# Optimization experiments

Measured on AMD Instinct MI355X. Metric: run time of the kernel, lower is better.

Reference implementation:

```python
import jax, jax.numpy as jnp
import numpy as np

N = 2048
IMG_H = 128
IMG_W = 128
FX = 160.0
FY = 160.0
CX = IMG_W / 2.0
CY = IMG_H / 2.0
THRESH = 0.001  # matches thresh in tile_based_vol_rendering
EPS = 1e-6


def _quat_scale_to_rotmat(q, s):
    # qsvec2rotmat_batched: R(q) @ diag(s), q = (w, x, y, z)
    q = q / jnp.linalg.norm(q, axis=-1, keepdims=True)
    w, x, y, z = q[..., 0], q[..., 1], q[..., 2], q[..., 3]
    R = jnp.stack([
        jnp.stack([1 - 2 * (y * y + z * z), 2 * (x * y - w * z), 2 * (x * z + w * y)], -1),
        jnp.stack([2 * (x * y + w * z), 1 - 2 * (x * x + z * z), 2 * (y * z - w * x)], -1),
        jnp.stack([2 * (x * z - w * y), 2 * (y * z + w * x), 1 - 2 * (x * x + y * y)], -1),
    ], -2)  # [N,3,3]
    return R * s[:, None, :]  # scale columns


def _jacobian(u):
    # EWA projection Jacobian, exactly as in the torch code
    l = jnp.linalg.norm(u, axis=-1)
    x, y, z = u[..., 0], u[..., 1], u[..., 2]
    zero = jnp.zeros_like(z)
    row0 = jnp.stack([1.0 / z, zero, -x / (z * z)], -1)
    row1 = jnp.stack([zero, 1.0 / z, -y / (z * z)], -1)
    row2 = jnp.stack([x / l, y / l, z / l], -1)
    return jnp.stack([row0, row1, row2], -2)  # [N,3,3]


def _forward(mean, qvec, svec, color, alpha, c2w, H, W):
    # --- project_gaussians ---
    d = -c2w[:, 3]
    Wm = c2w[:, :3].T  # world->cam rotation
    pm = jnp.einsum('ij,bj->bi', Wm, mean + d)  # [N,3] camera-space means
    M = _quat_scale_to_rotmat(qvec, svec)
    sigma = jnp.einsum('bij,bkj->bik', M, M)  # R S S^T R^T
    J = _jacobian(pm)
    JW = jnp.einsum('bij,jk->bik', J, Wm)
    cov3 = jnp.einsum('bij,bjk,blk->bil', JW, sigma, JW)
    cov2d = cov3[:, :2, :2]  # [N,2,2]
    depth = pm[:, 2]
    mean2d = pm[:, :2] / depth[:, None]  # [N,2] camera-plane coords

    # --- global depth sort (replaces per-tile radix sort; same compositing order) ---
    order = jnp.argsort(depth)
    mean2d = jnp.take(mean2d, order, axis=0)
    cov2d = jnp.take(cov2d, order, axis=0)
    color_s = jnp.take(color, order, axis=0)
    alpha_s = jnp.take(alpha, order, axis=0)

    # --- 2x2 inverse covariance ---
    a = cov2d[:, 0, 0] + EPS
    b = cov2d[:, 0, 1]
    dd = cov2d[:, 1, 1] + EPS
    det = a * dd - b * b
    i00 = dd / det
    i01 = -b / det
    i11 = a / det

    # --- pixel centers on camera plane: topleft + pixel_size * (idx + 0.5) ---
    xs = (jnp.arange(W, dtype=mean.dtype) + 0.5) / FX - CX / FX  # [W]
    ys = (jnp.arange(H, dtype=mean.dtype) + 0.5) / FY - CY / FY  # [H]
    px = jnp.broadcast_to(xs[None, :], (H, W)).reshape(-1)  # [P]
    py = jnp.broadcast_to(ys[:, None], (H, W)).reshape(-1)  # [P]

    # --- sorted alpha compositing, dense per (pixel, gaussian) ---
    dx = px[:, None] - mean2d[None, :, 0]  # [P,N]
    dy = py[:, None] - mean2d[None, :, 1]  # [P,N]
    power = -0.5 * (i00[None, :] * dx * dx + 2.0 * i01[None, :] * dx * dy + i11[None, :] * dy * dy)
    wgt = alpha_s[None, :] * jnp.exp(power)  # [P,N]
    wgt = jnp.minimum(wgt, 0.999)
    wgt = jnp.where(wgt > THRESH, wgt, 0.0)  # CUDA kernel skip threshold
    T = jnp.cumprod(1.0 - wgt, axis=1)
    T = jnp.concatenate([jnp.ones((T.shape[0], 1), T.dtype), T[:, :-1]], axis=1)  # exclusive transmittance
    out = (wgt * T) @ color_s  # [P,3]
    return out.reshape(H, W, 3)


def setup_inputs() -> dict:
    key = jax.random.key(0)
    k1, k2, k3, k4, k5, k6 = jax.random.split(key, 6)
    z = jax.random.uniform(k1, (N,), minval=2.0, maxval=6.0)
    xy = jax.random.uniform(k2, (N, 2), minval=-0.3, maxval=0.3) * z[:, None]
    mean = jnp.concatenate([xy, z[:, None]], axis=-1).astype(jnp.float32)
    qvec = jax.random.normal(k3, (N, 4), dtype=jnp.float32)
    svec = jax.random.uniform(k4, (N, 3), minval=0.02, maxval=0.08, dtype=jnp.float32)
    color = jax.random.uniform(k5, (N, 3), dtype=jnp.float32)
    alpha = jax.random.uniform(k6, (N,), minval=0.3, maxval=0.9, dtype=jnp.float32)
    c2w = jnp.concatenate([jnp.eye(3, dtype=jnp.float32), jnp.zeros((3, 1), jnp.float32)], axis=-1)
    return {"mean": mean, "qvec": qvec, "svec": svec, "color": color,
            "alpha": alpha, "c2w": c2w, "H": IMG_H, "W": IMG_W}


def reference(mean, qvec, svec, color, alpha, c2w, H, W):
    return _forward(mean, qvec, svec, color, alpha, c2w, H, W)
```

## Files before the change

### kernel.cpp

```cpp
#include <hip/hip_runtime.h>

#define FXc 160.0f
#define FYc 160.0f
#define THRESHc 0.001f
#define EPSc 1e-6f
#define QTH 1024
#define CAP 1000

__global__ __launch_bounds__(QTH) void fused_kernel(
    const float* __restrict__ mean, const float* __restrict__ qvec,
    const float* __restrict__ svec, const float* __restrict__ color,
    const float* __restrict__ alpha, const float* __restrict__ c2w,
    const int* __restrict__ Wp, const int* __restrict__ Hp,
    float* __restrict__ out, int n) {
    __shared__ unsigned long long key[CAP];
    __shared__ int   ord[CAP];
    __shared__ float4 pp0[CAP], pp1[CAP];
    __shared__ float  ppa[CAP];
    __shared__ float4 partial[16][64];
    __shared__ int cntS;

    int tid = threadIdx.x;
    int lane = tid & 63;
    int w = tid >> 6;

    int W = *Wp, H = *Hp;
    int qpx = (W + 7) >> 3;
    int q = blockIdx.x;
    int qx = q % qpx, qy = q / qpx;
    float cxofx = (W * 0.5f) / FXc, cyofy = (H * 0.5f) / FYc;
    float wx0 = ((float)(qx*8)   + 0.5f) / FXc - cxofx;
    float wx1 = ((float)(qx*8+7) + 0.5f) / FXc - cxofx;
    float wy0 = ((float)(qy*8)   + 0.5f) / FYc - cyofy;
    float wy1 = ((float)(qy*8+7) + 0.5f) / FYc - cyofy;
    int col = qx * 8 + (lane & 7);
    int row = qy * 8 + (lane >> 3);
    float px = ((float)col + 0.5f) / FXc - cxofx;
    float py = ((float)row + 0.5f) / FYc - cyofy;

    if (tid == 0) cntS = 0;
    __syncthreads();

    float tx = c2w[3], ty = c2w[7], tz = c2w[11];
    float W00 = c2w[0], W01 = c2w[4], W02 = c2w[8];
    float W10 = c2w[1], W11 = c2w[5], W12 = c2w[9];
    float W20 = c2w[2], W21 = c2w[6], W22 = c2w[10];

    for (int base = 0; base < n; base += QTH) {
        int i = base + tid;
        bool hit = false;
        float m2x = 0.f, m2y = 0.f, h00 = 0.f, h01 = 0.f, h11 = 0.f;
        float cr = 0.f, cg = 0.f, cb = 0.f, al = 0.f, pmz = 0.f;
        if (i < n) {
            al = alpha[i];
            if (al > THRESHc) {
                float mx = mean[3*i+0] - tx, my = mean[3*i+1] - ty, mz = mean[3*i+2] - tz;
                float pmx = W00*mx + W01*my + W02*mz;
                float pmy = W10*mx + W11*my + W12*mz;
                pmz = W20*mx + W21*my + W22*mz;
                float qw = qvec[4*i+0], qxx = qvec[4*i+1], qyy = qvec[4*i+2], qzz = qvec[4*i+3];
                float qinv = rsqrtf(qw*qw + qxx*qxx + qyy*qyy + qzz*qzz);
                qw *= qinv; qxx *= qinv; qyy *= qinv; qzz *= qinv;
                float R00 = 1.0f - 2.0f*(qyy*qyy + qzz*qzz), R01 = 2.0f*(qxx*qyy - qw*qzz), R02 = 2.0f*(qxx*qzz + qw*qyy);
                float R10 = 2.0f*(qxx*qyy + qw*qzz), R11 = 1.0f - 2.0f*(qxx*qxx + qzz*qzz), R12 = 2.0f*(qyy*qzz - qw*qxx);
                float R20 = 2.0f*(qxx*qzz - qw*qyy), R21 = 2.0f*(qyy*qzz + qw*qxx), R22 = 1.0f - 2.0f*(qxx*qxx + qyy*qyy);
                float sx = svec[3*i+0], sy = svec[3*i+1], sz = svec[3*i+2];
                float M00 = R00*sx, M01 = R01*sy, M02 = R02*sz;
                float M10 = R10*sx, M11 = R11*sy, M12 = R12*sz;
                float M20 = R20*sx, M21 = R21*sy, M22 = R22*sz;
                float iz = 1.0f / pmz, iz2 = iz*iz;
                float axx = pmx*iz2, ayy = pmy*iz2;
                float A0 = iz*W00 - axx*W20, A1 = iz*W01 - axx*W21, A2 = iz*W02 - axx*W22;
                float B0 = iz*W10 - ayy*W20, B1 = iz*W11 - ayy*W21, B2 = iz*W12 - ayy*W22;
                float V00 = A0*M00 + A1*M10 + A2*M20;
                float V01 = A0*M01 + A1*M11 + A2*M21;
                float V02 = A0*M02 + A1*M12 + A2*M22;
                float V10 = B0*M00 + B1*M10 + B2*M20;
                float V11 = B0*M01 + B1*M11 + B2*M21;
                float V12 = B0*M02 + B1*M12 + B2*M22;
                float a  = V00*V00 + V01*V01 + V02*V02 + EPSc;
                float bb = V00*V10 + V01*V11 + V02*V12;
                float dd = V10*V10 + V11*V11 + V12*V12 + EPSc;
                float det  = a*dd - bb*bb;
                float idet = 1.0f / det;
                h00 = -0.5f * dd * idet;
                h01 =  bb * idet;
                h11 = -0.5f * a  * idet;
                m2x = pmx*iz; m2y = pmy*iz;
                float cc = logf(al / THRESHc);
                float ex = sqrtf(2.0f*cc*a)  * 1.0009f + 1e-6f;
                float ey = sqrtf(2.0f*cc*dd) * 1.0009f + 1e-6f;
                hit = !(m2x + ex < wx0 || m2x - ex > wx1 ||
                        m2y + ey < wy0 || m2y - ey > wy1);
                if (hit) { cr = color[3*i+0]; cg = color[3*i+1]; cb = color[3*i+2]; }
            }
        }
        unsigned long long mb = __ballot(hit);
        if (mb) {
            int leader = __builtin_ctzll(mb);
            int cw = (int)__popcll(mb);
            int basep = 0;
            if (lane == leader) basep = atomicAdd(&cntS, cw);
            basep = __shfl(basep, leader);
            if (hit) {
                int slot = basep + (int)__popcll(mb & ((1ull << lane) - 1ull));
                if (slot < CAP) {
                    unsigned fb = __float_as_uint(pmz);
                    fb = (fb & 0x80000000u) ? ~fb : (fb | 0x80000000u);
                    key[slot] = ((unsigned long long)fb << 32) | (unsigned)i;
                    pp0[slot] = make_float4(m2x, m2y, h00, h01);
                    pp1[slot] = make_float4(h11, cr, cg, cb);
                    ppa[slot] = al;
                }
            }
        }
    }
    __syncthreads();
    int c = min(cntS, CAP);

    for (int k = tid; k < c; k += QTH) {
        unsigned long long e = key[k];
        int pos = 0;
        for (int m = 0; m < c; ++m) pos += (key[m] < e);
        ord[pos] = k;
    }
    __syncthreads();

    int sl = (c + 15) >> 4;
    int b0 = min(c, w * sl), b1 = min(c, b0 + sl);
    float T = 1.0f, r = 0.0f, g = 0.0f, b = 0.0f;
    for (int j = b0; j < b1; ++j) {
        int s = ord[j];
        float4 a0 = pp0[s];
        float4 a1 = pp1[s];
        float  al = ppa[s];
        float dx = px - a0.x;
        float dy = py - a0.y;
        float pw = dx * (a0.z * dx + a0.w * dy) + a1.x * dy * dy;
        float ww = al * __expf(pw);
        ww = fminf(ww, 0.999f);
        ww = (ww > THRESHc) ? ww : 0.0f;
        float wT = ww * T;
        r = fmaf(wT, a1.y, r);
        g = fmaf(wT, a1.z, g);
        b = fmaf(wT, a1.w, b);
        T = T - wT;
    }
    partial[w][lane] = make_float4(r, g, b, T);
    __syncthreads();

    if (w == 0) {
        float Tf = 1.0f, rf = 0.0f, gf = 0.0f, bf = 0.0f;
#pragma unroll
        for (int s = 0; s < 16; ++s) {
            float4 v = partial[s][lane];
            rf = fmaf(Tf, v.x, rf);
            gf = fmaf(Tf, v.y, gf);
            bf = fmaf(Tf, v.z, bf);
            Tf *= v.w;
        }
        if (col < W && row < H) {
            int p = row * W + col;
            out[3*p+0] = rf;
            out[3*p+1] = gf;
            out[3*p+2] = bf;
        }
    }
}

extern "C" void kernel_launch(void* const* d_in, const int* in_sizes, int n_in,
                              void* d_out, int out_size, void* d_ws, size_t ws_size,
                              hipStream_t stream) {
    const float* mean  = (const float*)d_in[0];
    const float* qvec  = (const float*)d_in[1];
    const float* svec  = (const float*)d_in[2];
    const float* color = (const float*)d_in[3];
    const float* alpha = (const float*)d_in[4];
    const float* c2w   = (const float*)d_in[5];
    const int*   Hp    = (const int*)d_in[6];
    const int*   Wp    = (const int*)d_in[7];
    float* out = (float*)d_out;

    int n = in_sizes[0] / 3;
    int npix = out_size / 3;
    int Wh = 128;
    int Hh = npix / Wh;
    int quads = ((Wh + 7) / 8) * ((Hh + 7) / 8);

    fused_kernel<<<quads, QTH, 0, stream>>>(mean, qvec, svec, color, alpha, c2w,
                                            Wp, Hp, out, n);
}
```

Before: 16.32 us.

## Add conservative scale-bound prefilter before full covariance projection per tile

Splits culling into two passes: a cheap conservative bound using the max scale squared (an isotropic covariance upper bound) to find candidate Gaussians per 8x8 tile, then the full quaternion/covariance computation only for candidates. This avoids computing the full 2D covariance for all N Gaussians in each of the 256 blocks. It adds a candidate list in shared memory (capped at 2048) and an extra barrier. It also switches to fast log/sqrt intrinsics and a vectorized quaternion load. If candidates exceed the cap, results would silently be dropped.

```diff
diff --git a/kernel.cpp b/kernel.cpp
--- a/kernel.cpp
+++ b/kernel.cpp
@@ -5,7 +5,8 @@
 #define THRESHc 0.001f
 #define EPSc 1e-6f
 #define QTH 1024
-#define CAP 1000
+#define CAP 1024
+#define CCAP 2048
 
 __global__ __launch_bounds__(QTH) void fused_kernel(
     const float* __restrict__ mean, const float* __restrict__ qvec,
@@ -18,7 +19,8 @@
     __shared__ float4 pp0[CAP], pp1[CAP];
     __shared__ float  ppa[CAP];
     __shared__ float4 partial[16][64];
-    __shared__ int cntS;
+    __shared__ int   cand[CCAP];
+    __shared__ int cntS, candS;
 
     int tid = threadIdx.x;
     int lane = tid & 63;
@@ -38,7 +40,7 @@
     float px = ((float)col + 0.5f) / FXc - cxofx;
     float py = ((float)row + 0.5f) / FYc - cyofy;
 
-    if (tid == 0) cntS = 0;
+    if (tid == 0) { cntS = 0; candS = 0; }
     __syncthreads();
 
     float tx = c2w[3], ty = c2w[7], tz = c2w[11];
@@ -48,52 +50,93 @@
 
     for (int base = 0; base < n; base += QTH) {
         int i = base + tid;
-        bool hit = false;
-        float m2x = 0.f, m2y = 0.f, h00 = 0.f, h01 = 0.f, h11 = 0.f;
-        float cr = 0.f, cg = 0.f, cb = 0.f, al = 0.f, pmz = 0.f;
+        bool cd = false;
         if (i < n) {
-            al = alpha[i];
+            float al = alpha[i];
             if (al > THRESHc) {
                 float mx = mean[3*i+0] - tx, my = mean[3*i+1] - ty, mz = mean[3*i+2] - tz;
                 float pmx = W00*mx + W01*my + W02*mz;
                 float pmy = W10*mx + W11*my + W12*mz;
-                pmz = W20*mx + W21*my + W22*mz;
-                float qw = qvec[4*i+0], qxx = qvec[4*i+1], qyy = qvec[4*i+2], qzz = qvec[4*i+3];
-                float qinv = rsqrtf(qw*qw + qxx*qxx + qyy*qyy + qzz*qzz);
-                qw *= qinv; qxx *= qinv; qyy *= qinv; qzz *= qinv;
-                float R00 = 1.0f - 2.0f*(qyy*qyy + qzz*qzz), R01 = 2.0f*(qxx*qyy - qw*qzz), R02 = 2.0f*(qxx*qzz + qw*qyy);
-                float R10 = 2.0f*(qxx*qyy + qw*qzz), R11 = 1.0f - 2.0f*(qxx*qxx + qzz*qzz), R12 = 2.0f*(qyy*qzz - qw*qxx);
-                float R20 = 2.0f*(qxx*qzz - qw*qyy), R21 = 2.0f*(qyy*qzz + qw*qxx), R22 = 1.0f - 2.0f*(qxx*qxx + qyy*qyy);
+                float pmz = W20*mx + W21*my + W22*mz;
                 float sx = svec[3*i+0], sy = svec[3*i+1], sz = svec[3*i+2];
-                float M00 = R00*sx, M01 = R01*sy, M02 = R02*sz;
-                float M10 = R10*sx, M11 = R11*sy, M12 = R12*sz;
-                float M20 = R20*sx, M21 = R21*sy, M22 = R22*sz;
+                float smax = fmaxf(sx, fmaxf(sy, sz));
+                float s2 = smax * smax;
                 float iz = 1.0f / pmz, iz2 = iz*iz;
-                float axx = pmx*iz2, ayy = pmy*iz2;
-                float A0 = iz*W00 - axx*W20, A1 = iz*W01 - axx*W21, A2 = iz*W02 - axx*W22;
-                float B0 = iz*W10 - ayy*W20, B1 = iz*W11 - ayy*W21, B2 = iz*W12 - ayy*W22;
-                float V00 = A0*M00 + A1*M10 + A2*M20;
-                float V01 = A0*M01 + A1*M11 + A2*M21;
-                float V02 = A0*M02 + A1*M12 + A2*M22;
-                float V10 = B0*M00 + B1*M10 + B2*M20;
-                float V11 = B0*M01 + B1*M11 + B2*M21;
-                float V12 = B0*M02 + B1*M12 + B2*M22;
-                float a  = V00*V00 + V01*V01 + V02*V02 + EPSc;
-                float bb = V00*V10 + V01*V11 + V02*V12;
-                float dd = V10*V10 + V11*V11 + V12*V12 + EPSc;
-                float det  = a*dd - bb*bb;
-                float idet = 1.0f / det;
-                h00 = -0.5f * dd * idet;
-                h01 =  bb * idet;
-                h11 = -0.5f * a  * idet;
-                m2x = pmx*iz; m2y = pmy*iz;
-                float cc = logf(al / THRESHc);
-                float ex = sqrtf(2.0f*cc*a)  * 1.0009f + 1e-6f;
-                float ey = sqrtf(2.0f*cc*dd) * 1.0009f + 1e-6f;
-                hit = !(m2x + ex < wx0 || m2x - ex > wx1 ||
-                        m2y + ey < wy0 || m2y - ey > wy1);
-                if (hit) { cr = color[3*i+0]; cg = color[3*i+1]; cb = color[3*i+2]; }
+                float ax = pmx*iz2, ay = pmy*iz2;
+                float ab = s2*(iz2 + ax*ax) + EPSc;
+                float db = s2*(iz2 + ay*ay) + EPSc;
+                float cc = __logf(al * (1.0f / THRESHc));
+                float exb = __builtin_sqrtf(2.0f*cc*ab) * 1.003f + 2e-6f;
+                float eyb = __builtin_sqrtf(2.0f*cc*db) * 1.003f + 2e-6f;
+                float m2x = pmx*iz, m2y = pmy*iz;
+                cd = !(m2x + exb < wx0 || m2x - exb > wx1 ||
+                       m2y + eyb < wy0 || m2y - eyb > wy1);
             }
+        }
+        unsigned long long mb = __ballot(cd);
+        if (mb) {
+            int leader = __builtin_ctzll(mb);
+            int cw = (int)__popcll(mb);
+            int basep = 0;
+            if (lane == leader) basep = atomicAdd(&candS, cw);
+            basep = __shfl(basep, leader);
+            if (cd) {
+                int slot = basep + (int)__popcll(mb & ((1ull << lane) - 1ull));
+                if (slot < CCAP) cand[slot] = i;
+            }
+        }
+    }
+    __syncthreads();
+    int nc = min(candS, CCAP);
+
+    for (int base = 0; base < nc; base += QTH) {
+        int k = base + tid;
+        bool hit = false;
+        float m2x = 0.f, m2y = 0.f, h00 = 0.f, h01 = 0.f, h11 = 0.f;
+        float al = 0.f, pmz = 0.f;
+        int i = 0;
+        if (k < nc) {
+            i = cand[k];
+            al = alpha[i];
+            float mx = mean[3*i+0] - tx, my = mean[3*i+1] - ty, mz = mean[3*i+2] - tz;
+            float pmx = W00*mx + W01*my + W02*mz;
+            float pmy = W10*mx + W11*my + W12*mz;
+            pmz = W20*mx + W21*my + W22*mz;
+            float4 qv = ((const float4*)qvec)[i];
+            float qw = qv.x, qxx = qv.y, qyy = qv.z, qzz = qv.w;
+            float qinv = rsqrtf(qw*qw + qxx*qxx + qyy*qyy + qzz*qzz);
+            qw *= qinv; qxx *= qinv; qyy *= qinv; qzz *= qinv;
+            float R00 = 1.0f - 2.0f*(qyy*qyy + qzz*qzz), R01 = 2.0f*(qxx*qyy - qw*qzz), R02 = 2.0f*(qxx*qzz + qw*qyy);
+            float R10 = 2.0f*(qxx*qyy + qw*qzz), R11 = 1.0f - 2.0f*(qxx*qxx + qzz*qzz), R12 = 2.0f*(qyy*qzz - qw*qxx);
+            float R20 = 2.0f*(qxx*qzz - qw*qyy), R21 = 2.0f*(qyy*qzz + qw*qxx), R22 = 1.0f - 2.0f*(qxx*qxx + qyy*qyy);
+            float sx = svec[3*i+0], sy = svec[3*i+1], sz = svec[3*i+2];
+            float M00 = R00*sx, M01 = R01*sy, M02 = R02*sz;
+            float M10 = R10*sx, M11 = R11*sy, M12 = R12*sz;
+            float M20 = R20*sx, M21 = R21*sy, M22 = R22*sz;
+            float iz = 1.0f / pmz, iz2 = iz*iz;
+            float axx = pmx*iz2, ayy = pmy*iz2;
+            float A0 = iz*W00 - axx*W20, A1 = iz*W01 - axx*W21, A2 = iz*W02 - axx*W22;
+            float B0 = iz*W10 - ayy*W20, B1 = iz*W11 - ayy*W21, B2 = iz*W12 - ayy*W22;
+            float V00 = A0*M00 + A1*M10 + A2*M20;
+            float V01 = A0*M01 + A1*M11 + A2*M21;
+            float V02 = A0*M02 + A1*M12 + A2*M22;
+            float V10 = B0*M00 + B1*M10 + B2*M20;
+            float V11 = B0*M01 + B1*M11 + B2*M21;
+            float V12 = B0*M02 + B1*M12 + B2*M22;
+            float a  = V00*V00 + V01*V01 + V02*V02 + EPSc;
+            float bb = V00*V10 + V01*V11 + V02*V12;
+            float dd = V10*V10 + V11*V11 + V12*V12 + EPSc;
+            float det  = a*dd - bb*bb;
+            float idet = 1.0f / det;
+            h00 = -0.5f * dd * idet;
+            h01 =  bb * idet;
+            h11 = -0.5f * a  * idet;
+            m2x = pmx*iz; m2y = pmy*iz;
+            float cc = __logf(al * (1.0f / THRESHc));
+            float ex = __builtin_sqrtf(2.0f*cc*a)  * 1.0009f + 1e-6f;
+            float ey = __builtin_sqrtf(2.0f*cc*dd) * 1.0009f + 1e-6f;
+            hit = !(m2x + ex < wx0 || m2x - ex > wx1 ||
+                    m2y + ey < wy0 || m2y - ey > wy1);
         }
         unsigned long long mb = __ballot(hit);
         if (mb) {
@@ -109,7 +152,7 @@
                     fb = (fb & 0x80000000u) ? ~fb : (fb | 0x80000000u);
                     key[slot] = ((unsigned long long)fb << 32) | (unsigned)i;
                     pp0[slot] = make_float4(m2x, m2y, h00, h01);
-                    pp1[slot] = make_float4(h11, cr, cg, cb);
+                    pp1[slot] = make_float4(h11, color[3*i+0], color[3*i+1], color[3*i+2]);
                     ppa[slot] = al;
                 }
             }
```

Result: faster. 14.81 us (-9.2%).
